# Performance work log

Hardware: AMD Instinct MI355X
Metric: run time of the kernel (lower is better)

Reference implementation:

```python
import jax, jax.numpy as jnp
import numpy as np

MARGIN = 0.2

def _sq_pdist(x):
    # squared euclidean pairwise distances, [N, N]
    r = jnp.sum(x * x, axis=-1)
    d2 = r[:, None] + r[None, :] - 2.0 * (x @ x.T)
    return jnp.maximum(d2, 0.0)

def setup_inputs() -> dict:
    key = jax.random.key(0)
    k1, k2, k3 = jax.random.split(key, 3)
    N, D, C = 384, 128, 32
    feat = jax.random.normal(k1, (N, D), dtype=jnp.float32)
    logits = jax.random.normal(k2, (N, C), dtype=jnp.float32)
    y = jax.random.randint(k3, (N,), 0, C, dtype=jnp.int64)
    return {"feat": feat, "logits": logits, "y": y}

def reference(feat, logits, y):
    # logits unused, kept for compatibility with the original signature
    d2 = _sq_pdist(feat)  # [N, N] squared distances (loss uses dist**2)
    same = y[:, None] == y[None, :]              # [N, N]
    n = y.shape[0]
    not_self = ~jnp.eye(n, dtype=bool)
    pos_mask = same & not_self                    # valid (anchor, positive)
    neg_mask = ~same                              # valid (anchor, negative)
    # BatchAll: every triplet (a, p, n) with pos_mask[a,p] and neg_mask[a,n]
    trip = jax.nn.relu(d2[:, :, None] - d2[:, None, :] + MARGIN)  # [N, N, N]
    valid = pos_mask[:, :, None] & neg_mask[:, None, :]           # [N, N, N]
    total = jnp.sum(jnp.where(valid, trip, 0.0))
    count = jnp.sum(valid.astype(jnp.float32))
    return total / count  # size_average=True -> mean over all triplets
```

## Files before the change

kernel.cpp:

```cpp
#include <hip/hip_runtime.h>

#define N 384
#define D 128
#define TLMARGIN 0.2f

__global__ __launch_bounds__(256) void transpose_kernel(const float* __restrict__ feat,
                                                        float* __restrict__ featT) {
    __shared__ float tile[32][33];
    const int jx = threadIdx.x;
    const int ty = threadIdx.y;
    const int j0 = blockIdx.x * 32;
    const int d0 = blockIdx.y * 32;
    #pragma unroll
    for (int k = 0; k < 4; ++k) {
        int jj = ty + 8 * k;
        tile[jj][jx] = feat[(j0 + jj) * D + d0 + jx];
    }
    __syncthreads();
    #pragma unroll
    for (int k = 0; k < 4; ++k) {
        int dd = ty + 8 * k;
        featT[(d0 + dd) * N + j0 + jx] = tile[jx][dd];
    }
}

__global__ __launch_bounds__(N) void triplet_main(const float* __restrict__ feat,
                                                  const float* __restrict__ featT,
                                                  const int* __restrict__ y,
                                                  float* __restrict__ ws,
                                                  float* __restrict__ out) {
    __shared__ float sfa[D];
    __shared__ float sd2[N];
    __shared__ int   plist[96];
    __shared__ int   pcount;
    __shared__ float swsum[N / 64];

    const int a = blockIdx.x;
    const int t = threadIdx.x;
    const int ya = y[a];
    const int yt = y[t];

    if (t < D) sfa[t] = feat[a * D + t];
    if (t == 0) pcount = 0;
    __syncthreads();

    const float* ft = featT + t;
    float s0 = 0.f, s1 = 0.f, s2 = 0.f, s3 = 0.f;
    #pragma unroll 8
    for (int d = 0; d < D; d += 4) {
        float x0 = sfa[d + 0] - ft[(d + 0) * N];
        float x1 = sfa[d + 1] - ft[(d + 1) * N];
        float x2 = sfa[d + 2] - ft[(d + 2) * N];
        float x3 = sfa[d + 3] - ft[(d + 3) * N];
        s0 = fmaf(x0, x0, s0);
        s1 = fmaf(x1, x1, s1);
        s2 = fmaf(x2, x2, s2);
        s3 = fmaf(x3, x3, s3);
    }
    sd2[t] = (s0 + s1) + (s2 + s3);

    if (t != a && yt == ya) {
        int idx = atomicAdd(&pcount, 1);
        plist[idx] = t;
    }
    __syncthreads();

    const int np = pcount;
    float acc = 0.f;
    if (yt != ya) {
        const float dn = sd2[t] - TLMARGIN;
        for (int i = 0; i < np; ++i) {
            float v = sd2[plist[i]] - dn;
            acc += fmaxf(v, 0.f);
        }
    }

    #pragma unroll
    for (int off = 32; off > 0; off >>= 1)
        acc += __shfl_down(acc, off);
    if ((t & 63) == 0) swsum[t >> 6] = acc;
    __syncthreads();

    if (t == 0) {
        float bs = 0.f;
        #pragma unroll
        for (int w = 0; w < N / 64; ++w) bs += swsum[w];
        const int nneg = N - np - 1;
        atomicAdd(&ws[0], bs);
        atomicAdd(&ws[1], (float)(np * nneg));
        __threadfence();
        unsigned int old = atomicAdd((unsigned int*)&ws[2], 1u);
        if (old == (unsigned int)(gridDim.x - 1)) {
            float tot = atomicAdd(&ws[0], 0.f);
            float cnt = atomicAdd(&ws[1], 0.f);
            out[0] = tot / cnt;
        }
    }
}

extern "C" void kernel_launch(void* const* d_in, const int* in_sizes, int n_in,
                              void* d_out, int out_size, void* d_ws, size_t ws_size,
                              hipStream_t stream) {
    const float* feat = (const float*)d_in[0];
    const int* y = (const int*)d_in[2];
    float* ws = (float*)d_ws;
    float* featT = ws + 16;
    float* out = (float*)d_out;

    hipMemsetAsync(d_ws, 0, 16, stream);
    transpose_kernel<<<dim3(12, 4), dim3(32, 8), 0, stream>>>(feat, featT);
    triplet_main<<<N, N, 0, stream>>>(feat, featT, y, ws, out);
}
```

Measured before the change: 79.21 us.

## Compute pairwise distance matrix with tiled kernel and drop memset launch

After: 77.88 us. Within noise of the previous version (-1.7%).

```diff
diff --git a/kernel.cpp b/kernel.cpp
--- a/kernel.cpp
+++ b/kernel.cpp
@@ -3,33 +3,55 @@
 #define N 384
 #define D 128
 #define TLMARGIN 0.2f
+#define TS 32
 
-__global__ __launch_bounds__(256) void transpose_kernel(const float* __restrict__ feat,
-                                                        float* __restrict__ featT) {
-    __shared__ float tile[32][33];
-    const int jx = threadIdx.x;
-    const int ty = threadIdx.y;
-    const int j0 = blockIdx.x * 32;
-    const int d0 = blockIdx.y * 32;
+
+__global__ __launch_bounds__(256) void d2_kernel(const float* __restrict__ feat,
+                                                 float* __restrict__ ws) {
+    __shared__ float As[TS][D + 1];
+    __shared__ float Bs[TS][D + 1];
+
+    const int t = threadIdx.x;
+    const int i0 = blockIdx.x * TS;
+    const int j0 = blockIdx.y * TS;
+
+    if (blockIdx.x == 0 && blockIdx.y == 0 && t < 4) ws[t] = 0.f;
+
     #pragma unroll
-    for (int k = 0; k < 4; ++k) {
-        int jj = ty + 8 * k;
-        tile[jj][jx] = feat[(j0 + jj) * D + d0 + jx];
+    for (int k = 0; k < 16; ++k) {
+        const int f = t + 256 * k;
+        const int r = f >> 7, c = f & 127;
+        As[r][c] = feat[(i0 + r) * D + c];
+        Bs[r][c] = feat[(j0 + r) * D + c];
     }
     __syncthreads();
-    #pragma unroll
-    for (int k = 0; k < 4; ++k) {
-        int dd = ty + 8 * k;
-        featT[(d0 + dd) * N + j0 + jx] = tile[jx][dd];
+
+    const int tj = t & 31;
+    const int ti0 = (t >> 5) << 2;
+    float a0 = 0.f, a1 = 0.f, a2 = 0.f, a3 = 0.f;
+    #pragma unroll 4
+    for (int d = 0; d < D; ++d) {
+        const float b = Bs[tj][d];
+        const float x0 = As[ti0 + 0][d] - b;
+        const float x1 = As[ti0 + 1][d] - b;
+        const float x2 = As[ti0 + 2][d] - b;
+        const float x3 = As[ti0 + 3][d] - b;
+        a0 = fmaf(x0, x0, a0);
+        a1 = fmaf(x1, x1, a1);
+        a2 = fmaf(x2, x2, a2);
+        a3 = fmaf(x3, x3, a3);
     }
+
+    float* d2m = ws + 64;
+    d2m[(i0 + ti0 + 0) * N + j0 + tj] = a0;
+    d2m[(i0 + ti0 + 1) * N + j0 + tj] = a1;
+    d2m[(i0 + ti0 + 2) * N + j0 + tj] = a2;
+    d2m[(i0 + ti0 + 3) * N + j0 + tj] = a3;
 }
 
-__global__ __launch_bounds__(N) void triplet_main(const float* __restrict__ feat,
-                                                  const float* __restrict__ featT,
-                                                  const int* __restrict__ y,
-                                                  float* __restrict__ ws,
-                                                  float* __restrict__ out) {
-    __shared__ float sfa[D];
+__global__ __launch_bounds__(N) void triplet_kernel(const int* __restrict__ y,
+                                                    float* __restrict__ ws,
+                                                    float* __restrict__ out) {
     __shared__ float sd2[N];
     __shared__ int   plist[96];
     __shared__ int   pcount;
@@ -37,27 +59,13 @@
 
     const int a = blockIdx.x;
     const int t = threadIdx.x;
+    const float* d2m = ws + 64;
+
     const int ya = y[a];
     const int yt = y[t];
-
-    if (t < D) sfa[t] = feat[a * D + t];
+    sd2[t] = d2m[a * N + t];
     if (t == 0) pcount = 0;
     __syncthreads();
-
-    const float* ft = featT + t;
-    float s0 = 0.f, s1 = 0.f, s2 = 0.f, s3 = 0.f;
-    #pragma unroll 8
-    for (int d = 0; d < D; d += 4) {
-        float x0 = sfa[d + 0] - ft[(d + 0) * N];
-        float x1 = sfa[d + 1] - ft[(d + 1) * N];
-        float x2 = sfa[d + 2] - ft[(d + 2) * N];
-        float x3 = sfa[d + 3] - ft[(d + 3) * N];
-        s0 = fmaf(x0, x0, s0);
-        s1 = fmaf(x1, x1, s1);
-        s2 = fmaf(x2, x2, s2);
-        s3 = fmaf(x3, x3, s3);
-    }
-    sd2[t] = (s0 + s1) + (s2 + s3);
 
     if (t != a && yt == ya) {
         int idx = atomicAdd(&pcount, 1);
@@ -85,7 +93,7 @@
         float bs = 0.f;
         #pragma unroll
         for (int w = 0; w < N / 64; ++w) bs += swsum[w];
-        const int nneg = N - np - 1;
+        const int nneg = N - 1 - np;
         atomicAdd(&ws[0], bs);
         atomicAdd(&ws[1], (float)(np * nneg));
         __threadfence();
@@ -104,10 +112,8 @@
     const float* feat = (const float*)d_in[0];
     const int* y = (const int*)d_in[2];
     float* ws = (float*)d_ws;
-    float* featT = ws + 16;
     float* out = (float*)d_out;
 
-    hipMemsetAsync(d_ws, 0, 16, stream);
-    transpose_kernel<<<dim3(12, 4), dim3(32, 8), 0, stream>>>(feat, featT);
-    triplet_main<<<N, N, 0, stream>>>(feat, featT, y, ws, out);
+    d2_kernel<<<dim3(N / TS, N / TS), 256, 0, stream>>>(feat, ws);
+    triplet_kernel<<<N, N, 0, stream>>>(y, ws, out);
 }
```
